# Kernel tuning notes

Measured on AMD Instinct MI355X. Metric: run time of the kernel, lower is better.

## Reference

```python
import jax, jax.numpy as jnp
import numpy as np

N_NODES = 100_000
N_EDGES = 1_600_000
N_GRAPHS = 512
D_IN = 128
D_H = 64
D_OUT = 32
N_CONV = 4  # n_layers - 1
BN_EPS = 1e-5


def setup_inputs() -> dict:
    key = jax.random.key(0)
    ks = jax.random.split(key, 10)
    h = jax.random.normal(ks[0], (N_NODES, D_IN), dtype=jnp.float32)
    src = jax.random.randint(ks[1], (N_EDGES,), 0, N_NODES, dtype=jnp.int32)
    dst = jax.random.randint(ks[2], (N_EDGES,), 0, N_NODES, dtype=jnp.int32)
    graph_ids = jnp.sort(jax.random.randint(ks[3], (N_NODES,), 0, N_GRAPHS, dtype=jnp.int32))
    s = 0.05
    fc1_w0 = jax.random.normal(ks[4], (D_IN, D_H), dtype=jnp.float32) * s
    fc1_w = jax.random.normal(ks[5], (N_CONV - 1, D_H, D_H), dtype=jnp.float32) * s
    fc2_w = jax.random.normal(ks[6], (N_CONV, D_H, D_H), dtype=jnp.float32) * s
    bn1_g = jnp.ones((N_CONV, D_H), dtype=jnp.float32)
    bn1_b = jnp.zeros((N_CONV, D_H), dtype=jnp.float32)
    bn2_g = jnp.ones((N_CONV, D_H), dtype=jnp.float32)
    bn2_b = jnp.zeros((N_CONV, D_H), dtype=jnp.float32)
    pred_w = jax.random.normal(ks[7], (N_CONV, D_H, D_OUT), dtype=jnp.float32) * s
    pred_b = jnp.zeros((N_CONV, D_OUT), dtype=jnp.float32)
    return {"h": h, "src": src, "dst": dst, "graph_ids": graph_ids,
            "fc1_w0": fc1_w0, "fc1_w": fc1_w, "fc2_w": fc2_w,
            "bn1_g": bn1_g, "bn1_b": bn1_b, "bn2_g": bn2_g, "bn2_b": bn2_b,
            "pred_w": pred_w, "pred_b": pred_b}


def _batch_norm(x, g, b):
    # PyTorch training-mode BN: batch mean, biased variance
    m = jnp.mean(x, axis=0)
    v = jnp.var(x, axis=0)
    return (x - m) * jax.lax.rsqrt(v + BN_EPS) * g + b


def reference(h, src, dst, graph_ids, fc1_w0, fc1_w, fc2_w,
              bn1_g, bn1_b, bn2_g, bn2_b, pred_w, pred_b):
    # GIN: h' = MLP((1+eps)*h + sum_{j in N(i)} h_j), eps=0 (learn_eps=False)
    score = jnp.zeros((N_GRAPHS, D_OUT), dtype=h.dtype)
    for l in range(N_CONV):
        agg = h + jax.ops.segment_sum(h[src], dst, num_segments=N_NODES)
        w1 = fc1_w0 if l == 0 else fc1_w[l - 1]
        # _MLP: fc2(relu(BN(fc1(x))))
        h = jax.nn.relu(_batch_norm(agg @ w1, bn1_g[l], bn1_b[l])) @ fc2_w[l]
        # outer BN + relu
        h = jax.nn.relu(_batch_norm(h, bn2_g[l], bn2_b[l]))
        # SumPooling per graph; readout skips layer-0 input rep, dropout is eval-mode identity
        pooled = jax.ops.segment_sum(h, graph_ids, num_segments=N_GRAPHS)
        score = score + pooled @ pred_w[l] + pred_b[l]
    return score
```

## Files before the change

kernel.cpp:

```cpp
#include <hip/hip_runtime.h>

#define N_NODES 100000
#define N_EDGES 1600000
#define N_GRAPHS 512
#define D_IN 128
#define D_H 64
#define D_OUT 32
#define N_CONV 4
#define BN_EPS 1e-5f
#define NSLOT 32

#define NB 512
#define NPB 196
#define NBUSED 511
#define CHUNK 8192
#define MAXE 4096

typedef unsigned short ushort_t;
typedef unsigned int uint_t;
typedef __attribute__((ext_vector_type(8))) short bf16x8;
typedef __attribute__((ext_vector_type(4))) float f32x4;
union U4B8 { uint4 u; bf16x8 v; };

__device__ inline float b2f(ushort_t u) {
    union { uint_t i; float f; } c; c.i = ((uint_t)u) << 16; return c.f;
}
__device__ inline ushort_t f2b(float f) {
    union { uint_t i; float f; } c; c.f = f;
    uint_t r = (c.i + 0x7fffu + ((c.i >> 16) & 1u)) >> 16;
    return (ushort_t)r;
}
__device__ inline float blo(uint_t v) { return b2f((ushort_t)(v & 0xffffu)); }
__device__ inline float bhi(uint_t v) { return b2f((ushort_t)(v >> 16)); }

__global__ __launch_bounds__(256) void zero_kernel(int* __restrict__ p, int nwords) {
    int i = blockIdx.x * 256 + threadIdx.x;
    if (i < nwords) p[i] = 0;
}

__global__ __launch_bounds__(256) void bucket_count(const int* __restrict__ dst,
                                                    int* __restrict__ bucketCnt) {
    __shared__ int l[NB];
    int t = threadIdx.x;
    for (int i = t; i < NB; i += 256) l[i] = 0;
    __syncthreads();
    long base = (long)blockIdx.x * 4096;
    for (int i = t; i < 4096; i += 256) {
        long e = base + i;
        if (e < N_EDGES) atomicAdd(&l[(unsigned)dst[e] / NPB], 1);
    }
    __syncthreads();
    for (int i = t; i < NB; i += 256) if (l[i]) atomicAdd(&bucketCnt[i], l[i]);
}

__global__ __launch_bounds__(512) void bucket_scan(const int* __restrict__ bucketCnt,
                                                   int* __restrict__ bucketOffs,
                                                   int* __restrict__ bucketCur) {
    __shared__ int s[512];
    int t = threadIdx.x;
    int v = bucketCnt[t];
    s[t] = v;
    __syncthreads();
    for (int off = 1; off < 512; off <<= 1) {
        int u = (t >= off) ? s[t - off] : 0;
        __syncthreads();
        s[t] += u;
        __syncthreads();
    }
    int excl = s[t] - v;
    bucketOffs[t] = excl;
    bucketCur[t] = excl;
    if (t == 511) bucketOffs[512] = s[511];
}

__global__ __launch_bounds__(256) void binned_scatter(const int* __restrict__ src,
                                                      const int* __restrict__ dst,
                                                      int* __restrict__ bucketCur,
                                                      uint2* __restrict__ pairs) {
    __shared__ uint2 sorted[CHUNK];
    __shared__ int lcnt[NB], loffs[NB], lcur[NB], gbase[NB];
    __shared__ int ps[256];
    int t = threadIdx.x;
    long e0 = (long)blockIdx.x * CHUNK;
    int nvalid = (int)min((long)CHUNK, (long)N_EDGES - e0);
    for (int i = t; i < NB; i += 256) lcnt[i] = 0;
    __syncthreads();
    for (int i = t; i < nvalid; i += 256)
        atomicAdd(&lcnt[(unsigned)dst[e0 + i] / NPB], 1);
    __syncthreads();
    int a0 = lcnt[2 * t], a1 = lcnt[2 * t + 1];
    ps[t] = a0 + a1;
    __syncthreads();
    for (int off = 1; off < 256; off <<= 1) {
        int u = (t >= off) ? ps[t - off] : 0;
        __syncthreads();
        ps[t] += u;
        __syncthreads();
    }
    int ex = ps[t] - (a0 + a1);
    loffs[2 * t] = ex; loffs[2 * t + 1] = ex + a0;
    lcur[2 * t] = ex;  lcur[2 * t + 1] = ex + a0;
    __syncthreads();
    for (int i = t; i < NB; i += 256) {
        int c = lcnt[i];
        gbase[i] = c ? atomicAdd(&bucketCur[i], c) : 0;
    }
    for (int i = t; i < nvalid; i += 256) {
        int d = dst[e0 + i];
        int b = (unsigned)d / NPB;
        int pos = atomicAdd(&lcur[b], 1);
        sorted[pos] = make_uint2((unsigned)src[e0 + i], (unsigned)d);
    }
    __syncthreads();
    for (int i = t; i < nvalid; i += 256) {
        uint2 pr = sorted[i];
        int b = pr.y / NPB;
        long gpos = (long)gbase[b] + (i - loffs[b]);
        pairs[gpos] = pr;
    }
}

__global__ __launch_bounds__(256) void csr_finalize(const uint2* __restrict__ pairs,
                                                    const int* __restrict__ bucketOffs,
                                                    int* __restrict__ offs,
                                                    int* __restrict__ csr) {
    __shared__ uint2 lp[MAXE];
    __shared__ int lsrc[MAXE];
    __shared__ int lcnt[NPB], lofs[NPB + 1], lcur[NPB];
    __shared__ int ls[256];
    int b = blockIdx.x, t = threadIdx.x;
    int e0 = bucketOffs[b], e1 = bucketOffs[b + 1];
    int ne = e1 - e0;
    int n0 = b * NPB;
    int nn = min(NPB, N_NODES - n0);
    for (int i = t; i < ne; i += 256) lp[i] = pairs[e0 + i];
    for (int i = t; i < nn; i += 256) lcnt[i] = 0;
    __syncthreads();
    for (int i = t; i < ne; i += 256) atomicAdd(&lcnt[lp[i].y - n0], 1);
    __syncthreads();
    int v = (t < nn) ? lcnt[t] : 0;
    ls[t] = v;
    __syncthreads();
    for (int off = 1; off < 256; off <<= 1) {
        int u = (t >= off) ? ls[t - off] : 0;
        __syncthreads();
        ls[t] += u;
        __syncthreads();
    }
    if (t < nn) { lofs[t] = ls[t] - v; lcur[t] = ls[t] - v; offs[n0 + t] = e0 + ls[t] - v; }
    if (t == 0 && b == NBUSED - 1) offs[N_NODES] = e1;
    __syncthreads();
    for (int i = t; i < ne; i += 256) {
        int pos = atomicAdd(&lcur[lp[i].y - n0], 1);
        lsrc[pos] = (int)lp[i].x;
    }
    __syncthreads();
    for (int i = t; i < ne; i += 256) csr[e0 + i] = lsrc[i];
}

#define SLABS 4
#define GEMM_BLOCKS 391
__global__ __launch_bounds__(256) void gemm0(const float* __restrict__ in,
                                             const float* __restrict__ w,
                                             ushort_t* __restrict__ y16) {
    __shared__ uint4 Bl[4][4][64];
    int t = threadIdx.x;
    for (int idx = t; idx < 4 * 4 * 64; idx += 256) {
        int l = idx & 63, nt = (idx >> 6) & 3, kk = idx >> 8;
        int k0 = kk * 32 + ((l >> 4) << 3), c = nt * 16 + (l & 15);
        uint4 o;
        o.x = (uint_t)f2b(w[(k0 + 0) * 64 + c]) | ((uint_t)f2b(w[(k0 + 1) * 64 + c]) << 16);
        o.y = (uint_t)f2b(w[(k0 + 2) * 64 + c]) | ((uint_t)f2b(w[(k0 + 3) * 64 + c]) << 16);
        o.z = (uint_t)f2b(w[(k0 + 4) * 64 + c]) | ((uint_t)f2b(w[(k0 + 5) * 64 + c]) << 16);
        o.w = (uint_t)f2b(w[(k0 + 6) * 64 + c]) | ((uint_t)f2b(w[(k0 + 7) * 64 + c]) << 16);
        Bl[kk][nt][l] = o;
    }
    __syncthreads();
    int wv = t >> 6, lane = t & 63, lq = lane >> 4, lr = lane & 15;
    bf16x8 B[4][4];
#pragma unroll
    for (int kk = 0; kk < 4; kk++)
#pragma unroll
        for (int nt = 0; nt < 4; nt++) { U4B8 cv; cv.u = Bl[kk][nt][lane]; B[kk][nt] = cv.v; }
    for (int s = 0; s < SLABS; s++) {
        long rb = ((long)blockIdx.x * SLABS + s) * 64 + wv * 16;
        long n = rb + lr;
        const float* rp = in + (n < N_NODES ? n : 0) * 128;
        f32x4 zero = {0.f, 0.f, 0.f, 0.f};
        f32x4 acc[4] = {zero, zero, zero, zero};
#pragma unroll
        for (int kk = 0; kk < 4; kk++) {
            float4 u = *(const float4*)(rp + kk * 32 + lq * 8);
            float4 v = *(const float4*)(rp + kk * 32 + lq * 8 + 4);
            bf16x8 a;
            a[0] = (short)f2b(u.x); a[1] = (short)f2b(u.y);
            a[2] = (short)f2b(u.z); a[3] = (short)f2b(u.w);
            a[4] = (short)f2b(v.x); a[5] = (short)f2b(v.y);
            a[6] = (short)f2b(v.z); a[7] = (short)f2b(v.w);
#pragma unroll
            for (int nt = 0; nt < 4; nt++)
                acc[nt] = __builtin_amdgcn_mfma_f32_16x16x32_bf16(a, B[kk][nt], acc[nt], 0, 0, 0);
        }
#pragma unroll
        for (int nt = 0; nt < 4; nt++)
#pragma unroll
            for (int j = 0; j < 4; j++) {
                long rr = rb + lq * 4 + j;
                if (rr < N_NODES) y16[rr * 64 + nt * 16 + lr] = f2b(acc[nt][j]);
            }
    }
}

template <bool OSTAT>
__global__ __launch_bounds__(256) void gemm_bn(const uint4* __restrict__ in,
                                               const float* __restrict__ w,
                                               const float* __restrict__ bnip,
                                               const float* __restrict__ gi,
                                               const float* __restrict__ bi,
                                               ushort_t* __restrict__ outY,
                                               float* __restrict__ ostat) {
    __shared__ uint4 Bl[2][4][64];
    __shared__ float sc[64], sh[64];
    __shared__ float red1[4][64], red2[4][64];
    int t = threadIdx.x;
    if (t < 64) {
        float S = 0.f, S2 = 0.f;
        for (int s = 0; s < NSLOT; s++) { S += bnip[s * 128 + t]; S2 += bnip[s * 128 + 64 + t]; }
        float mean = S * (1.f / N_NODES);
        float var = S2 * (1.f / N_NODES) - mean * mean;
        float r = rsqrtf(var + BN_EPS);
        float scv = gi[t] * r;
        sc[t] = scv; sh[t] = bi[t] - mean * scv;
    }
    for (int idx = t; idx < 2 * 4 * 64; idx += 256) {
        int l = idx & 63, nt = (idx >> 6) & 3, kk = idx >> 8;
        int k0 = kk * 32 + ((l >> 4) << 3), c = nt * 16 + (l & 15);
        uint4 o;
        o.x = (uint_t)f2b(w[(k0 + 0) * 64 + c]) | ((uint_t)f2b(w[(k0 + 1) * 64 + c]) << 16);
        o.y = (uint_t)f2b(w[(k0 + 2) * 64 + c]) | ((uint_t)f2b(w[(k0 + 3) * 64 + c]) << 16);
        o.z = (uint_t)f2b(w[(k0 + 4) * 64 + c]) | ((uint_t)f2b(w[(k0 + 5) * 64 + c]) << 16);
        o.w = (uint_t)f2b(w[(k0 + 6) * 64 + c]) | ((uint_t)f2b(w[(k0 + 7) * 64 + c]) << 16);
        Bl[kk][nt][l] = o;
    }
    __syncthreads();
    int wv = t >> 6, lane = t & 63, lq = lane >> 4, lr = lane & 15;
    bf16x8 B[2][4];
#pragma unroll
    for (int kk = 0; kk < 2; kk++)
#pragma unroll
        for (int nt = 0; nt < 4; nt++) { U4B8 cv; cv.u = Bl[kk][nt][lane]; B[kk][nt] = cv.v; }
    float s1[4] = {0.f, 0.f, 0.f, 0.f}, s2[4] = {0.f, 0.f, 0.f, 0.f};
    for (int s = 0; s < SLABS; s++) {
        long rb = ((long)blockIdx.x * SLABS + s) * 64 + wv * 16;
        long n = rb + lr;
        bool ok = n < N_NODES;
        const uint4* rp = in + (ok ? n : 0) * 8;
        f32x4 zero = {0.f, 0.f, 0.f, 0.f};
        f32x4 acc[4] = {zero, zero, zero, zero};
#pragma unroll
        for (int kk = 0; kk < 2; kk++) {
            bf16x8 a;
            if (ok) {
                uint4 v = rp[kk * 4 + lq];
                int k0 = kk * 32 + lq * 8;
                float x0 = fmaxf(blo(v.x) * sc[k0 + 0] + sh[k0 + 0], 0.f);
                float x1 = fmaxf(bhi(v.x) * sc[k0 + 1] + sh[k0 + 1], 0.f);
                float x2 = fmaxf(blo(v.y) * sc[k0 + 2] + sh[k0 + 2], 0.f);
                float x3 = fmaxf(bhi(v.y) * sc[k0 + 3] + sh[k0 + 3], 0.f);
                float x4 = fmaxf(blo(v.z) * sc[k0 + 4] + sh[k0 + 4], 0.f);
                float x5 = fmaxf(bhi(v.z) * sc[k0 + 5] + sh[k0 + 5], 0.f);
                float x6 = fmaxf(blo(v.w) * sc[k0 + 6] + sh[k0 + 6], 0.f);
                float x7 = fmaxf(bhi(v.w) * sc[k0 + 7] + sh[k0 + 7], 0.f);
                a[0] = (short)f2b(x0); a[1] = (short)f2b(x1);
                a[2] = (short)f2b(x2); a[3] = (short)f2b(x3);
                a[4] = (short)f2b(x4); a[5] = (short)f2b(x5);
                a[6] = (short)f2b(x6); a[7] = (short)f2b(x7);
            } else {
#pragma unroll
                for (int j = 0; j < 8; j++) a[j] = 0;
            }
#pragma unroll
            for (int nt = 0; nt < 4; nt++)
                acc[nt] = __builtin_amdgcn_mfma_f32_16x16x32_bf16(a, B[kk][nt], acc[nt], 0, 0, 0);
        }
#pragma unroll
        for (int nt = 0; nt < 4; nt++)
#pragma unroll
            for (int j = 0; j < 4; j++) {
                long rr = rb + lq * 4 + j;
                float val = acc[nt][j];
                if (rr < N_NODES) outY[rr * 64 + nt * 16 + lr] = f2b(val);
                if (OSTAT) { s1[nt] += val; s2[nt] += val * val; }
            }
    }
    if (OSTAT) {
#pragma unroll
        for (int nt = 0; nt < 4; nt++) {
            s1[nt] += __shfl_xor(s1[nt], 16); s1[nt] += __shfl_xor(s1[nt], 32);
            s2[nt] += __shfl_xor(s2[nt], 16); s2[nt] += __shfl_xor(s2[nt], 32);
        }
        if (lq == 0) {
#pragma unroll
            for (int nt = 0; nt < 4; nt++) {
                red1[wv][nt * 16 + lr] = s1[nt];
                red2[wv][nt * 16 + lr] = s2[nt];
            }
        }
        __syncthreads();
        if (t < 64) {
            float S = red1[0][t] + red1[1][t] + red1[2][t] + red1[3][t];
            float S2 = red2[0][t] + red2[1][t] + red2[2][t] + red2[3][t];
            int slot = blockIdx.x & (NSLOT - 1);
            atomicAdd(&ostat[slot * 128 + t], S);
            atomicAdd(&ostat[slot * 128 + 64 + t], S2);
        }
    }
}

__global__ __launch_bounds__(256) void aggregate(const uint_t* __restrict__ y32,
                                                 const int* __restrict__ offs,
                                                 const int* __restrict__ csr,
                                                 uint_t* __restrict__ aggOut,
                                                 float* __restrict__ bn1p) {
    int t = threadIdx.x;
    int wv = t >> 6, lane = t & 63;
    int g = lane >> 3, l = lane & 7;
    __shared__ float l1[4][64], l2[4][64];
    float st1[8], st2[8];
#pragma unroll
    for (int m = 0; m < 8; m++) { st1[m] = 0.f; st2[m] = 0.f; }
    int nb_base = blockIdx.x * 32 + wv * 8;
    for (int j = 0; j < 8; j++) {
        int n = nb_base + j;
        if (n >= N_NODES) break;
        int p0 = offs[n], p1 = offs[n + 1];
        int cnt = 1 + (p1 - p0);
        int rounds = (cnt + 7) >> 3;
        float accA[4] = {0.f, 0.f, 0.f, 0.f}, accB[4] = {0.f, 0.f, 0.f, 0.f};
        int e = g;
        int idx = (e == 0) ? n : ((e < cnt) ? csr[p0 + e - 1] : -1);
        for (int r = 0; r < rounds; r++) {
            int ne = e + 8;
            int nidx = (r + 1 < rounds && ne < cnt) ? csr[p0 + ne - 1] : -1;
            if (idx >= 0) {
                uint4 v = *(const uint4*)(y32 + (long)idx * 32 + 4 * l);
                accA[0] += __uint_as_float(v.x << 16);
                accB[0] += __uint_as_float(v.x & 0xffff0000u);
                accA[1] += __uint_as_float(v.y << 16);
                accB[1] += __uint_as_float(v.y & 0xffff0000u);
                accA[2] += __uint_as_float(v.z << 16);
                accB[2] += __uint_as_float(v.z & 0xffff0000u);
                accA[3] += __uint_as_float(v.w << 16);
                accB[3] += __uint_as_float(v.w & 0xffff0000u);
            }
            e = ne; idx = nidx;
        }
#pragma unroll
        for (int m = 0; m < 4; m++) {
            accA[m] += __shfl_xor(accA[m], 8);
            accB[m] += __shfl_xor(accB[m], 8);
            accA[m] += __shfl_xor(accA[m], 16);
            accB[m] += __shfl_xor(accB[m], 16);
            accA[m] += __shfl_xor(accA[m], 32);
            accB[m] += __shfl_xor(accB[m], 32);
        }
        if (g == 0) {
            uint4 o;
            o.x = (uint_t)f2b(accA[0]) | ((uint_t)f2b(accB[0]) << 16);
            o.y = (uint_t)f2b(accA[1]) | ((uint_t)f2b(accB[1]) << 16);
            o.z = (uint_t)f2b(accA[2]) | ((uint_t)f2b(accB[2]) << 16);
            o.w = (uint_t)f2b(accA[3]) | ((uint_t)f2b(accB[3]) << 16);
            *(uint4*)&aggOut[(long)n * 32 + 4 * l] = o;
            st1[0] += accA[0]; st2[0] += accA[0] * accA[0];
            st1[1] += accB[0]; st2[1] += accB[0] * accB[0];
            st1[2] += accA[1]; st2[2] += accA[1] * accA[1];
            st1[3] += accB[1]; st2[3] += accB[1] * accB[1];
            st1[4] += accA[2]; st2[4] += accA[2] * accA[2];
            st1[5] += accB[2]; st2[5] += accB[2] * accB[2];
            st1[6] += accA[3]; st2[6] += accA[3] * accA[3];
            st1[7] += accB[3]; st2[7] += accB[3] * accB[3];
        }
    }
    if (g == 0) {
#pragma unroll
        for (int m = 0; m < 8; m++) { l1[wv][8 * l + m] = st1[m]; l2[wv][8 * l + m] = st2[m]; }
    }
    __syncthreads();
    if (t < 64) {
        float S = l1[0][t] + l1[1][t] + l1[2][t] + l1[3][t];
        float S2 = l2[0][t] + l2[1][t] + l2[2][t] + l2[3][t];
        int slot = blockIdx.x & (NSLOT - 1);
        atomicAdd(&bn1p[slot * 128 + t], S);
        atomicAdd(&bn1p[slot * 128 + 64 + t], S2);
    }
}

__global__ __launch_bounds__(256) void bn_pool(const uint_t* __restrict__ h2,
                                               const float* __restrict__ bn2p,
                                               const float* __restrict__ g2,
                                               const float* __restrict__ b2,
                                               const int* __restrict__ gid,
                                               float* __restrict__ pooled) {
    __shared__ float sc[64], sh[64];
    int t = threadIdx.x;
    if (t < 64) {
        float S = 0.f, S2 = 0.f;
        for (int s = 0; s < NSLOT; s++) { S += bn2p[s * 128 + t]; S2 += bn2p[s * 128 + 64 + t]; }
        float mean = S * (1.f / N_NODES);
        float var = S2 * (1.f / N_NODES) - mean * mean;
        float r = rsqrtf(var + BN_EPS);
        float scv = g2[t] * r;
        sc[t] = scv; sh[t] = b2[t] - mean * scv;
    }
    __syncthreads();
    int c = t & 31, rs = t >> 5;
    float sA = sc[2 * c], hA = sh[2 * c], sB = sc[2 * c + 1], hB = sh[2 * c + 1];
    long base = (long)blockIdx.x * 256;
    float pa = 0.f, pb2 = 0.f; int gc = -1;
    for (int i = 0; i < 32; i++) {
        long n = base + rs + 8 * i;
        if (n >= N_NODES) break;
        int g = gid[n];
        uint_t v = h2[n * 32 + c];
        float x0 = fmaxf(blo(v) * sA + hA, 0.f);
        float x1 = fmaxf(bhi(v) * sB + hB, 0.f);
        if (g != gc) {
            if (gc >= 0) {
                atomicAdd(&pooled[(long)gc * 64 + 2 * c], pa);
                atomicAdd(&pooled[(long)gc * 64 + 2 * c + 1], pb2);
            }
            gc = g; pa = 0.f; pb2 = 0.f;
        }
        pa += x0; pb2 += x1;
    }
    if (gc >= 0) {
        atomicAdd(&pooled[(long)gc * 64 + 2 * c], pa);
        atomicAdd(&pooled[(long)gc * 64 + 2 * c + 1], pb2);
    }
}

__global__ __launch_bounds__(256) void score_kernel(const float* __restrict__ pooled,
                                                    const float* __restrict__ pw,
                                                    const float* __restrict__ pb,
                                                    float* __restrict__ out) {
    int idx = blockIdx.x * 256 + threadIdx.x;
    int g = idx >> 5, o = idx & 31;
    float acc = 0.f;
    for (int l = 0; l < N_CONV; l++) {
        acc += pb[l * 32 + o];
        const float* pr = pooled + (long)l * N_GRAPHS * 64 + (long)g * 64;
        const float* wr = pw + l * 64 * 32;
        for (int k = 0; k < 64; k++) acc += pr[k] * wr[k * 32 + o];
    }
    out[idx] = acc;
}

extern "C" void kernel_launch(void* const* d_in, const int* in_sizes, int n_in,
                              void* d_out, int out_size, void* d_ws, size_t ws_size,
                              hipStream_t stream) {
    const float* h     = (const float*)d_in[0];
    const int*   src   = (const int*)d_in[1];
    const int*   dst   = (const int*)d_in[2];
    const int*   gid   = (const int*)d_in[3];
    const float* fc1w0 = (const float*)d_in[4];
    const float* fc1w  = (const float*)d_in[5];
    const float* fc2w  = (const float*)d_in[6];
    const float* bn1g  = (const float*)d_in[7];
    const float* bn1b  = (const float*)d_in[8];
    const float* bn2g  = (const float*)d_in[9];
    const float* bn2b  = (const float*)d_in[10];
    const float* pw    = (const float*)d_in[11];
    const float* pb    = (const float*)d_in[12];
    float* out = (float*)d_out;

    char* ws = (char*)d_ws;
    uint_t*   AGG16   = (uint_t*)  (ws);
    uint2*    pairs   = (uint2*)   (ws);
    ushort_t* X16     = (ushort_t*)(ws + 25600000);
    ushort_t* Y16     = (ushort_t*)(ws + 38400000);
    float*    bnst    = (float*)   (ws + 51200000);
    float*    pooled  = (float*)   (ws + 51331072);
    int*   bucketCnt  = (int*)     (ws + 51855360);
    int*   bucketOffs = (int*)     (ws + 51857408);
    int*   bucketCur  = (int*)     (ws + 51859460);
    int*   offs       = (int*)     (ws + 51861508);
    int*   csr        = (int*)     (ws + 52261512);

    const int zwords = (51857408 - 51200000) / 4;
    zero_kernel<<<(zwords + 255) / 256, 256, 0, stream>>>((int*)bnst, zwords);

    bucket_count<<<(N_EDGES + 4095) / 4096, 256, 0, stream>>>(dst, bucketCnt);
    bucket_scan<<<1, 512, 0, stream>>>(bucketCnt, bucketOffs, bucketCur);
    binned_scatter<<<(N_EDGES + CHUNK - 1) / CHUNK, 256, 0, stream>>>(src, dst, bucketCur, pairs);
    csr_finalize<<<NBUSED, 256, 0, stream>>>(pairs, bucketOffs, offs, csr);

    for (int l = 0; l < N_CONV; l++) {
        float* bn1p = bnst + (long)l * 8192;
        float* bn2p = bn1p + 4096;
        float* pl = pooled + (long)l * N_GRAPHS * 64;
        if (l == 0) {
            gemm0<<<GEMM_BLOCKS, 256, 0, stream>>>(h, fc1w0, Y16);
        } else {
            float* bn2p_prev = bnst + (long)(l - 1) * 8192 + 4096;
            gemm_bn<false><<<GEMM_BLOCKS, 256, 0, stream>>>((const uint4*)X16,
                fc1w + (long)(l - 1) * 4096, bn2p_prev,
                bn2g + (l - 1) * 64, bn2b + (l - 1) * 64, Y16, (float*)nullptr);
        }
        aggregate<<<3125, 256, 0, stream>>>((const uint_t*)Y16, offs, csr, AGG16, bn1p);
        gemm_bn<true><<<GEMM_BLOCKS, 256, 0, stream>>>((const uint4*)AGG16,
            fc2w + (long)l * 4096, bn1p, bn1g + l * 64, bn1b + l * 64, X16, bn2p);
        bn_pool<<<391, 256, 0, stream>>>((const uint_t*)X16, bn2p, bn2g + l * 64,
                                         bn2b + l * 64, gid, pl);
    }
    score_kernel<<<64, 256, 0, stream>>>(pooled, pw, pb, out);
}
```

Baseline: 410.8 us.

## Split gathered features into four column-quarter planes for cache-friendly aggregation

The first GEMM of each layer now writes its bf16 output in four column-major quarter planes (16 features each) instead of row-major 64-wide rows. The aggregate kernel launches four times as many blocks; each block handles one quarter, gathering 32-byte rows across 32 neighbor slots per wave instead of 128-byte rows across 8 slots. The aim is to shrink the random-gather working set per pass so each quarter plane (about 3.2 MB) fits in cache, at the cost of re-reading CSR offsets and indices four times and doing more shuffle reductions.

```diff
diff --git a/kernel.cpp b/kernel.cpp
--- a/kernel.cpp
+++ b/kernel.cpp
@@ -206,7 +206,8 @@
 #pragma unroll
             for (int j = 0; j < 4; j++) {
                 long rr = rb + lq * 4 + j;
-                if (rr < N_NODES) y16[rr * 64 + nt * 16 + lr] = f2b(acc[nt][j]);
+                if (rr < N_NODES)
+                    y16[((long)nt * N_NODES + rr) * 16 + lr] = f2b(acc[nt][j]);
             }
     }
 }
@@ -289,7 +290,10 @@
             for (int j = 0; j < 4; j++) {
                 long rr = rb + lq * 4 + j;
                 float val = acc[nt][j];
-                if (rr < N_NODES) outY[rr * 64 + nt * 16 + lr] = f2b(val);
+                if (rr < N_NODES) {
+                    if (OSTAT) outY[rr * 64 + nt * 16 + lr] = f2b(val);
+                    else       outY[((long)nt * N_NODES + rr) * 16 + lr] = f2b(val);
+                }
                 if (OSTAT) { s1[nt] += val; s2[nt] += val * val; }
             }
     }
@@ -317,33 +321,35 @@
     }
 }
 
-__global__ __launch_bounds__(256) void aggregate(const uint_t* __restrict__ y32,
+__global__ __launch_bounds__(256) void aggregate(const uint_t* __restrict__ yq_all,
                                                  const int* __restrict__ offs,
                                                  const int* __restrict__ csr,
                                                  uint_t* __restrict__ aggOut,
                                                  float* __restrict__ bn1p) {
     int t = threadIdx.x;
     int wv = t >> 6, lane = t & 63;
-    int g = lane >> 3, l = lane & 7;
-    __shared__ float l1[4][64], l2[4][64];
+    int slot = lane >> 1, h = lane & 1;
+    int b = blockIdx.x;
+    int q = b & 3, chunk = b >> 2;
+    const uint_t* yq = yq_all + (long)q * N_NODES * 8;
+    __shared__ float l1[4][16], l2[4][16];
     float st1[8], st2[8];
 #pragma unroll
     for (int m = 0; m < 8; m++) { st1[m] = 0.f; st2[m] = 0.f; }
-    int nb_base = blockIdx.x * 32 + wv * 8;
+    int nb_base = chunk * 32 + wv * 8;
     for (int j = 0; j < 8; j++) {
         int n = nb_base + j;
-        if (n >= N_NODES) break;
         int p0 = offs[n], p1 = offs[n + 1];
         int cnt = 1 + (p1 - p0);
-        int rounds = (cnt + 7) >> 3;
+        int rounds = (cnt + 31) >> 5;
         float accA[4] = {0.f, 0.f, 0.f, 0.f}, accB[4] = {0.f, 0.f, 0.f, 0.f};
-        int e = g;
-        int idx = (e == 0) ? n : ((e < cnt) ? csr[p0 + e - 1] : -1);
+        int e = slot;
+        int idx = (slot == 0) ? n : ((slot < cnt) ? csr[p0 + slot - 1] : -1);
         for (int r = 0; r < rounds; r++) {
-            int ne = e + 8;
-            int nidx = (r + 1 < rounds && ne < cnt) ? csr[p0 + ne - 1] : -1;
+            int ne = e + 32;
+            int nidx = (ne < cnt) ? csr[p0 + ne - 1] : -1;
             if (idx >= 0) {
-                uint4 v = *(const uint4*)(y32 + (long)idx * 32 + 4 * l);
+                uint4 v = *(const uint4*)(yq + (long)idx * 8 + h * 4);
                 accA[0] += __uint_as_float(v.x << 16);
                 accB[0] += __uint_as_float(v.x & 0xffff0000u);
                 accA[1] += __uint_as_float(v.y << 16);
@@ -357,6 +363,10 @@
         }
 #pragma unroll
         for (int m = 0; m < 4; m++) {
+            accA[m] += __shfl_xor(accA[m], 2);
+            accB[m] += __shfl_xor(accB[m], 2);
+            accA[m] += __shfl_xor(accA[m], 4);
+            accB[m] += __shfl_xor(accB[m], 4);
             accA[m] += __shfl_xor(accA[m], 8);
             accB[m] += __shfl_xor(accB[m], 8);
             accA[m] += __shfl_xor(accA[m], 16);
@@ -364,13 +374,13 @@
             accA[m] += __shfl_xor(accA[m], 32);
             accB[m] += __shfl_xor(accB[m], 32);
         }
-        if (g == 0) {
+        if (slot == 0) {
             uint4 o;
             o.x = (uint_t)f2b(accA[0]) | ((uint_t)f2b(accB[0]) << 16);
             o.y = (uint_t)f2b(accA[1]) | ((uint_t)f2b(accB[1]) << 16);
             o.z = (uint_t)f2b(accA[2]) | ((uint_t)f2b(accB[2]) << 16);
             o.w = (uint_t)f2b(accA[3]) | ((uint_t)f2b(accB[3]) << 16);
-            *(uint4*)&aggOut[(long)n * 32 + 4 * l] = o;
+            *(uint4*)&aggOut[(long)n * 32 + q * 8 + h * 4] = o;
             st1[0] += accA[0]; st2[0] += accA[0] * accA[0];
             st1[1] += accB[0]; st2[1] += accB[0] * accB[0];
             st1[2] += accA[1]; st2[2] += accA[1] * accA[1];
@@ -381,17 +391,20 @@
             st1[7] += accB[3]; st2[7] += accB[3] * accB[3];
         }
     }
-    if (g == 0) {
-#pragma unroll
-        for (int m = 0; m < 8; m++) { l1[wv][8 * l + m] = st1[m]; l2[wv][8 * l + m] = st2[m]; }
-    }
-    __syncthreads();
-    if (t < 64) {
+    if (slot == 0) {
+#pragma unroll
+        for (int m = 0; m < 8; m++) {
+            l1[wv][h * 8 + m] = st1[m];
+            l2[wv][h * 8 + m] = st2[m];
+        }
+    }
+    __syncthreads();
+    if (t < 16) {
         float S = l1[0][t] + l1[1][t] + l1[2][t] + l1[3][t];
         float S2 = l2[0][t] + l2[1][t] + l2[2][t] + l2[3][t];
-        int slot = blockIdx.x & (NSLOT - 1);
-        atomicAdd(&bn1p[slot * 128 + t], S);
-        atomicAdd(&bn1p[slot * 128 + 64 + t], S2);
+        int slotc = blockIdx.x & (NSLOT - 1);
+        atomicAdd(&bn1p[slotc * 128 + q * 16 + t], S);
+        atomicAdd(&bn1p[slotc * 128 + 64 + q * 16 + t], S2);
     }
 }
 
@@ -506,7 +519,7 @@
                 fc1w + (long)(l - 1) * 4096, bn2p_prev,
                 bn2g + (l - 1) * 64, bn2b + (l - 1) * 64, Y16, (float*)nullptr);
         }
-        aggregate<<<3125, 256, 0, stream>>>((const uint_t*)Y16, offs, csr, AGG16, bn1p);
+        aggregate<<<3125 * 4, 256, 0, stream>>>((const uint_t*)Y16, offs, csr, AGG16, bn1p);
         gemm_bn<true><<<GEMM_BLOCKS, 256, 0, stream>>>((const uint4*)AGG16,
             fc2w + (long)l * 4096, bn1p, bn1g + l * 64, bn1b + l * 64, X16, bn2p);
         bn_pool<<<391, 256, 0, stream>>>((const uint_t*)X16, bn2p, bn2g + l * 64,
```

New measurement: 905.5 us. 120% more time.

## Pack edge pairs into 32 bits, prefetch gathers, grid-stride aggregate

Applied to the files above, without the earlier changes.

Edge pairs are packed into one 32-bit word (src shifted left 9, local dst offset in the low bits), with the bucket id kept in a separate LDS array. This halves the pair traffic between binned_scatter and csr_finalize and drops the divides. The aggregate kernel now loads the next neighbor row before accumulating the current one to overlap gather latency. It also runs a fixed grid of 2048 blocks striding over the 3125 node chunks, which gives fewer BN-stat atomics but leaves some blocks with two chunks and others with one.

```diff
diff --git a/kernel.cpp b/kernel.cpp
--- a/kernel.cpp
+++ b/kernel.cpp
@@ -15,6 +15,8 @@
 #define NBUSED 511
 #define CHUNK 8192
 #define MAXE 4096
+#define AGG_BLOCKS 2048
+#define AGG_CHUNKS 3125
 
 typedef unsigned short ushort_t;
 typedef unsigned int uint_t;
@@ -76,8 +78,9 @@
 __global__ __launch_bounds__(256) void binned_scatter(const int* __restrict__ src,
                                                       const int* __restrict__ dst,
                                                       int* __restrict__ bucketCur,
-                                                      uint2* __restrict__ pairs) {
-    __shared__ uint2 sorted[CHUNK];
+                                                      uint_t* __restrict__ pairs) {
+    __shared__ uint_t sortedp[CHUNK];
+    __shared__ ushort_t sbkt[CHUNK];
     __shared__ int lcnt[NB], loffs[NB], lcur[NB], gbase[NB];
     __shared__ int ps[256];
     int t = threadIdx.x;
@@ -109,24 +112,24 @@
         int d = dst[e0 + i];
         int b = (unsigned)d / NPB;
         int pos = atomicAdd(&lcur[b], 1);
-        sorted[pos] = make_uint2((unsigned)src[e0 + i], (unsigned)d);
+        sortedp[pos] = ((uint_t)src[e0 + i] << 9) | (uint_t)(d - b * NPB);
+        sbkt[pos] = (ushort_t)b;
     }
     __syncthreads();
     for (int i = t; i < nvalid; i += 256) {
-        uint2 pr = sorted[i];
-        int b = pr.y / NPB;
+        int b = sbkt[i];
         long gpos = (long)gbase[b] + (i - loffs[b]);
-        pairs[gpos] = pr;
-    }
-}
-
-__global__ __launch_bounds__(256) void csr_finalize(const uint2* __restrict__ pairs,
+        pairs[gpos] = sortedp[i];
+    }
+}
+
+__global__ __launch_bounds__(256) void csr_finalize(const uint_t* __restrict__ pairs,
                                                     const int* __restrict__ bucketOffs,
                                                     int* __restrict__ offs,
                                                     int* __restrict__ csr) {
-    __shared__ uint2 lp[MAXE];
+    __shared__ uint_t lp[MAXE];
     __shared__ int lsrc[MAXE];
-    __shared__ int lcnt[NPB], lofs[NPB + 1], lcur[NPB];
+    __shared__ int lcnt[NPB], lcur[NPB];
     __shared__ int ls[256];
     int b = blockIdx.x, t = threadIdx.x;
     int e0 = bucketOffs[b], e1 = bucketOffs[b + 1];
@@ -136,7 +139,7 @@
     for (int i = t; i < ne; i += 256) lp[i] = pairs[e0 + i];
     for (int i = t; i < nn; i += 256) lcnt[i] = 0;
     __syncthreads();
-    for (int i = t; i < ne; i += 256) atomicAdd(&lcnt[lp[i].y - n0], 1);
+    for (int i = t; i < ne; i += 256) atomicAdd(&lcnt[lp[i] & 511u], 1);
     __syncthreads();
     int v = (t < nn) ? lcnt[t] : 0;
     ls[t] = v;
@@ -147,12 +150,13 @@
         ls[t] += u;
         __syncthreads();
     }
-    if (t < nn) { lofs[t] = ls[t] - v; lcur[t] = ls[t] - v; offs[n0 + t] = e0 + ls[t] - v; }
+    if (t < nn) { lcur[t] = ls[t] - v; offs[n0 + t] = e0 + ls[t] - v; }
     if (t == 0 && b == NBUSED - 1) offs[N_NODES] = e1;
     __syncthreads();
     for (int i = t; i < ne; i += 256) {
-        int pos = atomicAdd(&lcur[lp[i].y - n0], 1);
-        lsrc[pos] = (int)lp[i].x;
+        uint_t p = lp[i];
+        int pos = atomicAdd(&lcur[p & 511u], 1);
+        lsrc[pos] = (int)(p >> 9);
     }
     __syncthreads();
     for (int i = t; i < ne; i += 256) csr[e0 + i] = lsrc[i];
@@ -329,56 +333,60 @@
     float st1[8], st2[8];
 #pragma unroll
     for (int m = 0; m < 8; m++) { st1[m] = 0.f; st2[m] = 0.f; }
-    int nb_base = blockIdx.x * 32 + wv * 8;
-    for (int j = 0; j < 8; j++) {
-        int n = nb_base + j;
-        if (n >= N_NODES) break;
-        int p0 = offs[n], p1 = offs[n + 1];
-        int cnt = 1 + (p1 - p0);
-        int rounds = (cnt + 7) >> 3;
-        float accA[4] = {0.f, 0.f, 0.f, 0.f}, accB[4] = {0.f, 0.f, 0.f, 0.f};
-        int e = g;
-        int idx = (e == 0) ? n : ((e < cnt) ? csr[p0 + e - 1] : -1);
-        for (int r = 0; r < rounds; r++) {
-            int ne = e + 8;
-            int nidx = (r + 1 < rounds && ne < cnt) ? csr[p0 + ne - 1] : -1;
-            if (idx >= 0) {
-                uint4 v = *(const uint4*)(y32 + (long)idx * 32 + 4 * l);
-                accA[0] += __uint_as_float(v.x << 16);
-                accB[0] += __uint_as_float(v.x & 0xffff0000u);
-                accA[1] += __uint_as_float(v.y << 16);
-                accB[1] += __uint_as_float(v.y & 0xffff0000u);
-                accA[2] += __uint_as_float(v.z << 16);
-                accB[2] += __uint_as_float(v.z & 0xffff0000u);
-                accA[3] += __uint_as_float(v.w << 16);
-                accB[3] += __uint_as_float(v.w & 0xffff0000u);
-            }
-            e = ne; idx = nidx;
-        }
-#pragma unroll
-        for (int m = 0; m < 4; m++) {
-            accA[m] += __shfl_xor(accA[m], 8);
-            accB[m] += __shfl_xor(accB[m], 8);
-            accA[m] += __shfl_xor(accA[m], 16);
-            accB[m] += __shfl_xor(accB[m], 16);
-            accA[m] += __shfl_xor(accA[m], 32);
-            accB[m] += __shfl_xor(accB[m], 32);
-        }
-        if (g == 0) {
-            uint4 o;
-            o.x = (uint_t)f2b(accA[0]) | ((uint_t)f2b(accB[0]) << 16);
-            o.y = (uint_t)f2b(accA[1]) | ((uint_t)f2b(accB[1]) << 16);
-            o.z = (uint_t)f2b(accA[2]) | ((uint_t)f2b(accB[2]) << 16);
-            o.w = (uint_t)f2b(accA[3]) | ((uint_t)f2b(accB[3]) << 16);
-            *(uint4*)&aggOut[(long)n * 32 + 4 * l] = o;
-            st1[0] += accA[0]; st2[0] += accA[0] * accA[0];
-            st1[1] += accB[0]; st2[1] += accB[0] * accB[0];
-            st1[2] += accA[1]; st2[2] += accA[1] * accA[1];
-            st1[3] += accB[1]; st2[3] += accB[1] * accB[1];
-            st1[4] += accA[2]; st2[4] += accA[2] * accA[2];
-            st1[5] += accB[2]; st2[5] += accB[2] * accB[2];
-            st1[6] += accA[3]; st2[6] += accA[3] * accA[3];
-            st1[7] += accB[3]; st2[7] += accB[3] * accB[3];
+    for (int chunk = blockIdx.x; chunk < AGG_CHUNKS; chunk += AGG_BLOCKS) {
+        int nb_base = chunk * 32 + wv * 8;
+        for (int j = 0; j < 8; j++) {
+            int n = nb_base + j;
+            int p0 = offs[n], p1 = offs[n + 1];
+            int cnt = 1 + (p1 - p0);
+            int rounds = (cnt + 7) >> 3;
+            float accA[4] = {0.f, 0.f, 0.f, 0.f}, accB[4] = {0.f, 0.f, 0.f, 0.f};
+            int e = g;
+            int idx = (g == 0) ? n : ((g < cnt) ? csr[p0 + g - 1] : -1);
+            uint4 v;
+            if (idx >= 0) v = *(const uint4*)(y32 + (long)idx * 32 + 4 * l);
+            for (int r = 0; r < rounds; r++) {
+                int ne = e + 8;
+                int nidx = (ne < cnt) ? csr[p0 + ne - 1] : -1;
+                uint4 vn;
+                if (nidx >= 0) vn = *(const uint4*)(y32 + (long)nidx * 32 + 4 * l);
+                if (idx >= 0) {
+                    accA[0] += __uint_as_float(v.x << 16);
+                    accB[0] += __uint_as_float(v.x & 0xffff0000u);
+                    accA[1] += __uint_as_float(v.y << 16);
+                    accB[1] += __uint_as_float(v.y & 0xffff0000u);
+                    accA[2] += __uint_as_float(v.z << 16);
+                    accB[2] += __uint_as_float(v.z & 0xffff0000u);
+                    accA[3] += __uint_as_float(v.w << 16);
+                    accB[3] += __uint_as_float(v.w & 0xffff0000u);
+                }
+                e = ne; idx = nidx; v = vn;
+            }
+#pragma unroll
+            for (int m = 0; m < 4; m++) {
+                accA[m] += __shfl_xor(accA[m], 8);
+                accB[m] += __shfl_xor(accB[m], 8);
+                accA[m] += __shfl_xor(accA[m], 16);
+                accB[m] += __shfl_xor(accB[m], 16);
+                accA[m] += __shfl_xor(accA[m], 32);
+                accB[m] += __shfl_xor(accB[m], 32);
+            }
+            if (g == 0) {
+                uint4 o;
+                o.x = (uint_t)f2b(accA[0]) | ((uint_t)f2b(accB[0]) << 16);
+                o.y = (uint_t)f2b(accA[1]) | ((uint_t)f2b(accB[1]) << 16);
+                o.z = (uint_t)f2b(accA[2]) | ((uint_t)f2b(accB[2]) << 16);
+                o.w = (uint_t)f2b(accA[3]) | ((uint_t)f2b(accB[3]) << 16);
+                *(uint4*)&aggOut[(long)n * 32 + 4 * l] = o;
+                st1[0] += accA[0]; st2[0] += accA[0] * accA[0];
+                st1[1] += accB[0]; st2[1] += accB[0] * accB[0];
+                st1[2] += accA[1]; st2[2] += accA[1] * accA[1];
+                st1[3] += accB[1]; st2[3] += accB[1] * accB[1];
+                st1[4] += accA[2]; st2[4] += accA[2] * accA[2];
+                st1[5] += accB[2]; st2[5] += accB[2] * accB[2];
+                st1[6] += accA[3]; st2[6] += accA[3] * accA[3];
+                st1[7] += accB[3]; st2[7] += accB[3] * accB[3];
+            }
         }
     }
     if (g == 0) {
@@ -475,7 +483,7 @@
 
     char* ws = (char*)d_ws;
     uint_t*   AGG16   = (uint_t*)  (ws);
-    uint2*    pairs   = (uint2*)   (ws);
+    uint_t*   pairs   = (uint_t*)  (ws);
     ushort_t* X16     = (ushort_t*)(ws + 25600000);
     ushort_t* Y16     = (ushort_t*)(ws + 38400000);
     float*    bnst    = (float*)   (ws + 51200000);
@@ -506,7 +514,7 @@
                 fc1w + (long)(l - 1) * 4096, bn2p_prev,
                 bn2g + (l - 1) * 64, bn2b + (l - 1) * 64, Y16, (float*)nullptr);
         }
-        aggregate<<<3125, 256, 0, stream>>>((const uint_t*)Y16, offs, csr, AGG16, bn1p);
+        aggregate<<<AGG_BLOCKS, 256, 0, stream>>>((const uint_t*)Y16, offs, csr, AGG16, bn1p);
         gemm_bn<true><<<GEMM_BLOCKS, 256, 0, stream>>>((const uint4*)AGG16,
             fc2w + (long)l * 4096, bn1p, bn1g + l * 64, bn1b + l * 64, X16, bn2p);
         bn_pool<<<391, 256, 0, stream>>>((const uint_t*)X16, bn2p, bn2g + l * 64,
```

Result: no change. 405.7 us (-1.2%).
